# Kernel optimization log

Measured on AMD Instinct MI355X. Metric: run time of the kernel, lower is better.

The kernel has to match this reference:

```python
import jax, jax.numpy as jnp
import numpy as np
from jax import lax

DIM = 192
HEADS = 4
HEAD_DIM = DIM // HEADS
B, H, W = 4, 256, 256
EPS = 1e-12


def _conv(x, w, groups=1):
    # NCHW / OIHW, stride 1, SAME padding
    return lax.conv_general_dilated(
        x, w, window_strides=(1, 1), padding='SAME',
        feature_group_count=groups,
        dimension_numbers=('NCHW', 'OIHW', 'NCHW'))


def setup_inputs() -> dict:
    key = jax.random.key(0)
    k1, k2, k3, k4 = jax.random.split(key, 4)
    x = jax.random.normal(k1, (B, DIM, H, W), dtype=jnp.float32)
    qkv_w = jax.random.normal(k2, (3 * DIM, DIM, 1, 1), dtype=jnp.float32) * (1.0 / np.sqrt(DIM))
    dw_w = jax.random.normal(k3, (3 * DIM, 1, 3, 3), dtype=jnp.float32) * (1.0 / 3.0)
    proj_w = jax.random.normal(k4, (DIM, DIM, 1, 1), dtype=jnp.float32) * (1.0 / np.sqrt(DIM))
    temperature = jnp.ones((HEADS, 1, 1), dtype=jnp.float32)
    return {'x': x, 'qkv_w': qkv_w, 'dw_w': dw_w, 'proj_w': proj_w,
            'temperature': temperature}


def reference(x, qkv_w, dw_w, proj_w, temperature):
    b, c, h, w = x.shape
    qkv = _conv(x, qkv_w)                    # [b, 3c, h, w] 1x1 conv
    qkv = _conv(qkv, dw_w, groups=3 * c)     # depthwise 3x3
    q, k, v = jnp.split(qkv, 3, axis=1)      # each [b, c, h, w]
    hw = h * w
    q = q.reshape(b, HEADS, HEAD_DIM, hw)
    k = k.reshape(b, HEADS, HEAD_DIM, hw)
    v = v.reshape(b, HEADS, HEAD_DIM, hw)
    # L2-normalize over spatial dim (F.normalize, eps=1e-12 via clamp_min)
    q = q / jnp.maximum(jnp.linalg.norm(q, axis=3, keepdims=True), EPS)
    k = k / jnp.maximum(jnp.linalg.norm(k, axis=3, keepdims=True), EPS)
    # channel-wise attention: [b, heads, head_dim, head_dim]
    attn = jnp.einsum('bhdn,bhen->bhde', q, k) * temperature[None]
    attn = jax.nn.softmax(attn, axis=3)
    out = jnp.einsum('bhde,bhen->bhdn', attn, v)  # [b, heads, head_dim, hw]
    out = out.reshape(b, c, h, w)
    return _conv(out, proj_w)
```

## Files before the change

kernel.cpp:

```cpp
#include <hip/hip_runtime.h>
#include <hip/hip_bf16.h>

#define BATCH 4
#define CDIM 192
#define HWDIM 65536
#define IMGW 256
#define NHEADS 4
#define HDIM 48
#define KPAD 200

typedef __attribute__((ext_vector_type(8))) short short8;
typedef __attribute__((ext_vector_type(4))) float f32x4;

#define MFMA16(a, b, c) __builtin_amdgcn_mfma_f32_16x16x32_bf16(a, b, c, 0, 0, 0)

__device__ __forceinline__ ushort f2bf(float x) {
    unsigned u = __float_as_uint(x);
    unsigned r = u + 0x7FFFu + ((u >> 16) & 1u);
    return (ushort)(r >> 16);
}
__device__ __forceinline__ float bf2f(ushort h) {
    return __uint_as_float(((unsigned)h) << 16);
}

__global__ __launch_bounds__(256) void wsplit(
    const float* __restrict__ in, ushort* __restrict__ hi, ushort* __restrict__ lo, int n)
{
    int i = blockIdx.x * 256 + threadIdx.x;
    if (i < n) {
        float x = in[i];
        ushort h = f2bf(x);
        hi[i] = h;
        lo[i] = f2bf(x - bf2f(h));
    }
}

template<bool SPLITOUT>
__global__ __launch_bounds__(256) void gemm_staged(
    const ushort* __restrict__ Ahi, const ushort* __restrict__ Alo,
    const float*  __restrict__ X,
    ushort* __restrict__ qk_out,
    float*  __restrict__ v_out,
    float*  __restrict__ plain)
{
    __shared__ __align__(16) ushort Bh[64][KPAD];
    __shared__ __align__(16) ushort Bl[64][KPAD];

    const int t    = threadIdx.x;
    const int lane = t & 63;
    const int wave = t >> 6;
    const int n0   = blockIdx.x * 64;
    const int mw   = blockIdx.y * 192 + wave * 48;
    const int ar   = lane & 15;
    const int kg   = (lane >> 4) * 8;

    {
        const int n4 = (t & 15) * 4;
        const int kb = (t >> 4) * 2;
#pragma unroll
        for (int pass = 0; pass < 6; ++pass) {
            const int k2 = pass * 32 + kb;
            float4 f0 = *(const float4*)(X + (size_t)k2 * HWDIM + n0 + n4);
            float4 f1 = *(const float4*)(X + (size_t)(k2 + 1) * HWDIM + n0 + n4);
            const float* a0 = (const float*)&f0;
            const float* a1 = (const float*)&f1;
#pragma unroll
            for (int i = 0; i < 4; ++i) {
                ushort h0 = f2bf(a0[i]);
                ushort l0 = f2bf(a0[i] - bf2f(h0));
                ushort h1 = f2bf(a1[i]);
                ushort l1 = f2bf(a1[i] - bf2f(h1));
                *(unsigned*)&Bh[n4 + i][k2] = (unsigned)h0 | ((unsigned)h1 << 16);
                *(unsigned*)&Bl[n4 + i][k2] = (unsigned)l0 | ((unsigned)l1 << 16);
            }
        }
    }
    __syncthreads();

    f32x4 acc[3][4];
#pragma unroll
    for (int i = 0; i < 3; ++i)
#pragma unroll
        for (int j = 0; j < 4; ++j) { f32x4 z = {0.f, 0.f, 0.f, 0.f}; acc[i][j] = z; }

    const ushort* aph = Ahi + (size_t)(mw + ar) * 192 + kg;
    const ushort* apl = Alo + (size_t)(mw + ar) * 192 + kg;

#pragma unroll
    for (int k0 = 0; k0 < 192; k0 += 32) {
        short8 ah[3], al[3], bh[4], bl[4];
#pragma unroll
        for (int i = 0; i < 3; ++i) {
            ah[i] = *reinterpret_cast<const short8*>(aph + i * 16 * 192 + k0);
            al[i] = *reinterpret_cast<const short8*>(apl + i * 16 * 192 + k0);
        }
#pragma unroll
        for (int j = 0; j < 4; ++j) {
            bh[j] = *reinterpret_cast<const short8*>(&Bh[j * 16 + ar][k0 + kg]);
            bl[j] = *reinterpret_cast<const short8*>(&Bl[j * 16 + ar][k0 + kg]);
        }
#pragma unroll
        for (int i = 0; i < 3; ++i)
#pragma unroll
            for (int j = 0; j < 4; ++j) {
                acc[i][j] = MFMA16(ah[i], bh[j], acc[i][j]);
                acc[i][j] = MFMA16(ah[i], bl[j], acc[i][j]);
                acc[i][j] = MFMA16(al[i], bh[j], acc[i][j]);
            }
    }

    const int rr = (lane >> 4) * 4;
#pragma unroll
    for (int i = 0; i < 3; ++i)
#pragma unroll
        for (int j = 0; j < 4; ++j) {
            const int n = n0 + j * 16 + (lane & 15);
#pragma unroll
            for (int r = 0; r < 4; ++r) {
                const int mm = mw + i * 16 + rr + r;
                const float v = acc[i][j][r];
                if (SPLITOUT) {
                    if (mm < 384) qk_out[(size_t)mm * HWDIM + n] = f2bf(v);
                    else          v_out[(size_t)(mm - 384) * HWDIM + n] = v;
                } else {
                    plain[(size_t)mm * HWDIM + n] = v;
                }
            }
        }
}

__global__ __launch_bounds__(256) void dw3x3_bf(
    const ushort* __restrict__ in,
    const float* __restrict__ wdw,
    ushort* __restrict__ out)
{
    const int ch = blockIdx.x;
    const int y0 = blockIdx.y * 8;
    const int x  = threadIdx.x;
    __shared__ float rows[10][258];
    const ushort* inc = in + (size_t)ch * HWDIM;
#pragma unroll
    for (int r = 0; r < 10; ++r) {
        const int y = y0 - 1 + r;
        rows[r][x + 1] = (y >= 0 && y < IMGW) ? bf2f(inc[y * IMGW + x]) : 0.f;
    }
    if (x < 10) { rows[x][0] = 0.f; rows[x][257] = 0.f; }
    __syncthreads();
    float w[9];
#pragma unroll
    for (int i = 0; i < 9; ++i) w[i] = wdw[ch * 9 + i];
#pragma unroll
    for (int r = 0; r < 8; ++r) {
        float s = 0.f;
#pragma unroll
        for (int dy = 0; dy < 3; ++dy)
#pragma unroll
            for (int dx = 0; dx < 3; ++dx)
                s = fmaf(rows[r + dy][x + dx], w[dy * 3 + dx], s);
        out[(size_t)ch * HWDIM + (y0 + r) * IMGW + x] = f2bf(s);
    }
}

__global__ __launch_bounds__(256) void dw3x3_f32(
    const float* __restrict__ in,
    const float* __restrict__ wdw,
    float* __restrict__ out)
{
    const int ch = blockIdx.x;
    const int y0 = blockIdx.y * 8;
    const int x  = threadIdx.x;
    __shared__ float rows[10][258];
    const float* inc = in + (size_t)ch * HWDIM;
#pragma unroll
    for (int r = 0; r < 10; ++r) {
        const int y = y0 - 1 + r;
        rows[r][x + 1] = (y >= 0 && y < IMGW) ? inc[y * IMGW + x] : 0.f;
    }
    if (x < 10) { rows[x][0] = 0.f; rows[x][257] = 0.f; }
    __syncthreads();
    float w[9];
#pragma unroll
    for (int i = 0; i < 9; ++i) w[i] = wdw[ch * 9 + i];
#pragma unroll
    for (int r = 0; r < 8; ++r) {
        float s = 0.f;
#pragma unroll
        for (int dy = 0; dy < 3; ++dy)
#pragma unroll
            for (int dx = 0; dx < 3; ++dx)
                s = fmaf(rows[r + dy][x + dx], w[dy * 3 + dx], s);
        out[(size_t)ch * HWDIM + (y0 + r) * IMGW + x] = s;
    }
}

__global__ __launch_bounds__(256) void gram_mfma(
    const ushort* __restrict__ qk,
    float* __restrict__ Sb)
{
    const int h = blockIdx.y;
    const int lane = threadIdx.x & 63;
    const int wave = threadIdx.x >> 6;
    const int nbase = blockIdx.x * 2048 + wave * 512;
    const ushort* q0  = qk + (size_t)(h * HDIM) * HWDIM;
    const ushort* k0p = qk + (size_t)(192 + h * HDIM) * HWDIM;
    const int ar = lane & 15;
    const int kg = (lane >> 4) * 8;

    f32x4 acc[3][3];
#pragma unroll
    for (int i = 0; i < 3; ++i)
#pragma unroll
        for (int j = 0; j < 3; ++j) { f32x4 z = {0.f, 0.f, 0.f, 0.f}; acc[i][j] = z; }
    float sq[3] = {0.f, 0.f, 0.f}, sk[3] = {0.f, 0.f, 0.f};

    for (int ks = 0; ks < 512; ks += 32) {
        const int n = nbase + ks + kg;
        short8 qa[3], ka[3];
#pragma unroll
        for (int i = 0; i < 3; ++i) {
            qa[i] = *reinterpret_cast<const short8*>(q0  + (size_t)(i * 16 + ar) * HWDIM + n);
            ka[i] = *reinterpret_cast<const short8*>(k0p + (size_t)(i * 16 + ar) * HWDIM + n);
        }
#pragma unroll
        for (int i = 0; i < 3; ++i)
#pragma unroll
            for (int e = 0; e < 8; ++e) {
                float fq = bf2f((ushort)qa[i][e]);
                float fk = bf2f((ushort)ka[i][e]);
                sq[i] = fmaf(fq, fq, sq[i]);
                sk[i] = fmaf(fk, fk, sk[i]);
            }
#pragma unroll
        for (int i = 0; i < 3; ++i)
#pragma unroll
            for (int j = 0; j < 3; ++j)
                acc[i][j] = MFMA16(qa[i], ka[j], acc[i][j]);
    }

    __shared__ float S_l[2400];
    for (int t = threadIdx.x; t < 2400; t += 256) S_l[t] = 0.f;
    __syncthreads();
    const int rr = (lane >> 4) * 4;
#pragma unroll
    for (int i = 0; i < 3; ++i)
#pragma unroll
        for (int j = 0; j < 3; ++j)
#pragma unroll
            for (int r = 0; r < 4; ++r)
                atomicAdd(&S_l[(i * 16 + rr + r) * 48 + (j * 16 + ar)], acc[i][j][r]);
#pragma unroll
    for (int i = 0; i < 3; ++i) {
        sq[i] += __shfl_xor(sq[i], 16); sq[i] += __shfl_xor(sq[i], 32);
        sk[i] += __shfl_xor(sk[i], 16); sk[i] += __shfl_xor(sk[i], 32);
    }
    if ((lane >> 4) == 0) {
#pragma unroll
        for (int i = 0; i < 3; ++i) {
            atomicAdd(&S_l[2304 + i * 16 + ar], sq[i]);
            atomicAdd(&S_l[2352 + i * 16 + ar], sk[i]);
        }
    }
    __syncthreads();
    float* Sg = Sb + h * 2400;
    for (int t = threadIdx.x; t < 2400; t += 256) atomicAdd(&Sg[t], S_l[t]);
}

__global__ __launch_bounds__(256) void attn_w2(
    const float* __restrict__ S,
    const float* __restrict__ proj,
    const float* __restrict__ temp,
    ushort* __restrict__ W2hi,
    ushort* __restrict__ W2lo)
{
    __shared__ float attn[NHEADS][HDIM][HDIM];
    __shared__ float nqs[NHEADS][HDIM], nks[NHEADS][HDIM];
    const int t = threadIdx.x;
    const int co0 = blockIdx.x * 48;
    for (int idx = t; idx < NHEADS * 96; idx += 256) {
        const int h = idx / 96, r = idx % 96;
        float v = sqrtf(S[h * 2400 + 2304 + r]);
        v = fmaxf(v, 1e-12f);
        if (r < 48) nqs[h][r] = v; else nks[h][r - 48] = v;
    }
    __syncthreads();
    if (t < NHEADS * HDIM) {
        const int h = t / HDIM, d = t % HDIM;
        const float tp  = temp[h];
        const float inq = 1.0f / nqs[h][d];
        float row[48];
        float mx = -1e30f;
#pragma unroll
        for (int e = 0; e < 48; ++e) {
            row[e] = S[h * 2400 + d * 48 + e] * inq / nks[h][e] * tp;
            mx = fmaxf(mx, row[e]);
        }
        float sum = 0.f;
#pragma unroll
        for (int e = 0; e < 48; ++e) { row[e] = expf(row[e] - mx); sum += row[e]; }
        const float isum = 1.0f / sum;
#pragma unroll
        for (int e = 0; e < 48; ++e) attn[h][d][e] = row[e] * isum;
    }
    __syncthreads();
    for (int idx = t; idx < 48 * 192; idx += 256) {
        const int co = co0 + idx / 192, he = idx % 192;
        const int h = he / 48, e = he % 48;
        const float* pr = proj + co * 192 + h * 48;
        float s = 0.f;
#pragma unroll
        for (int d = 0; d < 48; ++d) s = fmaf(pr[d], attn[h][d][e], s);
        ushort hh = f2bf(s);
        W2hi[co * 192 + he] = hh;
        W2lo[co * 192 + he] = f2bf(s - bf2f(hh));
    }
}

__global__ void zerof(float* __restrict__ p, int n)
{
    const int i = blockIdx.x * 256 + threadIdx.x;
    if (i < n) p[i] = 0.f;
}

extern "C" void kernel_launch(void* const* d_in, const int* in_sizes, int n_in,
                              void* d_out, int out_size, void* d_ws, size_t ws_size,
                              hipStream_t stream)
{
    const float* x      = (const float*)d_in[0];
    const float* qkv_w  = (const float*)d_in[1];
    const float* dw_w   = (const float*)d_in[2];
    const float* proj_w = (const float*)d_in[3];
    const float* temp   = (const float*)d_in[4];
    float* out = (float*)d_out;

    char* w = (char*)d_ws;
    ushort* qk_pre = (ushort*)w;                 w += (size_t)384 * HWDIM * 2;
    float*  v_pre  = (float*)w;                  w += (size_t)192 * HWDIM * 4;
    ushort* qk_dw  = (ushort*)w;                 w += (size_t)384 * HWDIM * 2;
    float*  v_dw   = (float*)w;                  w += (size_t)192 * HWDIM * 4;
    ushort* A1hi   = (ushort*)w;                 w += (size_t)576 * 192 * 2;
    ushort* A1lo   = (ushort*)w;                 w += (size_t)576 * 192 * 2;
    ushort* W2hi   = (ushort*)w;                 w += (size_t)192 * 192 * 2;
    ushort* W2lo   = (ushort*)w;                 w += (size_t)192 * 192 * 2;
    float*  S_all  = (float*)w;                  w += (size_t)BATCH * 4 * 2400 * 4;

    zerof<<<150, 256, 0, stream>>>(S_all, BATCH * 4 * 2400);
    wsplit<<<(576 * 192 + 255) / 256, 256, 0, stream>>>(qkv_w, A1hi, A1lo, 576 * 192);

    for (int b = 0; b < BATCH; ++b) {
        const float* xb = x   + (size_t)b * CDIM * HWDIM;
        float*       ob = out + (size_t)b * CDIM * HWDIM;
        float*       Sb = S_all + (size_t)b * 4 * 2400;

        gemm_staged<true><<<dim3(1024, 3), 256, 0, stream>>>(
            A1hi, A1lo, xb, qk_pre, v_pre, nullptr);
        dw3x3_bf <<<dim3(384, 32), 256, 0, stream>>>(qk_pre, dw_w, qk_dw);
        dw3x3_f32<<<dim3(192, 32), 256, 0, stream>>>(v_pre, dw_w + 384 * 9, v_dw);
        gram_mfma<<<dim3(32, 4), 256, 0, stream>>>(qk_dw, Sb);
        attn_w2<<<4, 256, 0, stream>>>(Sb, proj_w, temp, W2hi, W2lo);
        gemm_staged<false><<<dim3(1024, 1), 256, 0, stream>>>(
            W2hi, W2lo, v_dw, nullptr, nullptr, ob);
    }
}
```

Before: 1.256 ms.

## Batch two images per launch, swizzle GEMM LDS, vectorize depthwise conv

The pipeline now runs two batch images per launch through a z grid dimension, which halves the launch count and gives the small kernels (gram, attn_w2, proj GEMM) twice as many blocks. The GEMM's shared-memory B tile is stored with an XOR swizzle on 8-element chunks to reduce bank conflicts on the short8 reads. The two depthwise conv kernels become one template that loads with float4/ushort4 and computes a 4x4 output patch per thread over 16-row tiles. The cost is doubled workspace for intermediates.

New measurement: 1.078 ms. 14.2% less time.

```diff
diff --git a/kernel.cpp b/kernel.cpp
--- a/kernel.cpp
+++ b/kernel.cpp
@@ -2,6 +2,7 @@
 #include <hip/hip_bf16.h>
 
 #define BATCH 4
+#define ZPAIR 2
 #define CDIM 192
 #define HWDIM 65536
 #define IMGW 256
@@ -41,12 +42,14 @@
     const float*  __restrict__ X,
     ushort* __restrict__ qk_out,
     float*  __restrict__ v_out,
-    float*  __restrict__ plain)
-{
-    __shared__ __align__(16) ushort Bh[64][KPAD];
-    __shared__ __align__(16) ushort Bl[64][KPAD];
+    float*  __restrict__ plain,
+    int zAStride)
+{
+    __shared__ __align__(16) ushort Bh[64 * KPAD];
+    __shared__ __align__(16) ushort Bl[64 * KPAD];
 
     const int t    = threadIdx.x;
+    const int z    = blockIdx.z;
     const int lane = t & 63;
     const int wave = t >> 6;
     const int n0   = blockIdx.x * 64;
@@ -54,24 +57,30 @@
     const int ar   = lane & 15;
     const int kg   = (lane >> 4) * 8;
 
+    const float* Xz = X + (size_t)z * CDIM * HWDIM;
+
     {
         const int n4 = (t & 15) * 4;
         const int kb = (t >> 4) * 2;
 #pragma unroll
         for (int pass = 0; pass < 6; ++pass) {
             const int k2 = pass * 32 + kb;
-            float4 f0 = *(const float4*)(X + (size_t)k2 * HWDIM + n0 + n4);
-            float4 f1 = *(const float4*)(X + (size_t)(k2 + 1) * HWDIM + n0 + n4);
+            float4 f0 = *(const float4*)(Xz + (size_t)k2 * HWDIM + n0 + n4);
+            float4 f1 = *(const float4*)(Xz + (size_t)(k2 + 1) * HWDIM + n0 + n4);
             const float* a0 = (const float*)&f0;
             const float* a1 = (const float*)&f1;
+            const int cb = k2 >> 3;
+            const int ki = k2 & 7;
 #pragma unroll
             for (int i = 0; i < 4; ++i) {
+                const int row = n4 + i;
+                const int off = row * KPAD + ((cb ^ ((row >> 2) & 7)) << 3) + ki;
                 ushort h0 = f2bf(a0[i]);
                 ushort l0 = f2bf(a0[i] - bf2f(h0));
                 ushort h1 = f2bf(a1[i]);
                 ushort l1 = f2bf(a1[i] - bf2f(h1));
-                *(unsigned*)&Bh[n4 + i][k2] = (unsigned)h0 | ((unsigned)h1 << 16);
-                *(unsigned*)&Bl[n4 + i][k2] = (unsigned)l0 | ((unsigned)l1 << 16);
+                *(unsigned*)&Bh[off] = (unsigned)h0 | ((unsigned)h1 << 16);
+                *(unsigned*)&Bl[off] = (unsigned)l0 | ((unsigned)l1 << 16);
             }
         }
     }
@@ -81,10 +90,10 @@
 #pragma unroll
     for (int i = 0; i < 3; ++i)
 #pragma unroll
-        for (int j = 0; j < 4; ++j) { f32x4 z = {0.f, 0.f, 0.f, 0.f}; acc[i][j] = z; }
-
-    const ushort* aph = Ahi + (size_t)(mw + ar) * 192 + kg;
-    const ushort* apl = Alo + (size_t)(mw + ar) * 192 + kg;
+        for (int j = 0; j < 4; ++j) { f32x4 zz = {0.f, 0.f, 0.f, 0.f}; acc[i][j] = zz; }
+
+    const ushort* aph = Ahi + (size_t)z * zAStride + (size_t)(mw + ar) * 192 + kg;
+    const ushort* apl = Alo + (size_t)z * zAStride + (size_t)(mw + ar) * 192 + kg;
 
 #pragma unroll
     for (int k0 = 0; k0 < 192; k0 += 32) {
@@ -94,10 +103,13 @@
             ah[i] = *reinterpret_cast<const short8*>(aph + i * 16 * 192 + k0);
             al[i] = *reinterpret_cast<const short8*>(apl + i * 16 * 192 + k0);
         }
+        const int cb = (k0 + kg) >> 3;
 #pragma unroll
         for (int j = 0; j < 4; ++j) {
-            bh[j] = *reinterpret_cast<const short8*>(&Bh[j * 16 + ar][k0 + kg]);
-            bl[j] = *reinterpret_cast<const short8*>(&Bl[j * 16 + ar][k0 + kg]);
+            const int row = j * 16 + ar;
+            const int off = row * KPAD + ((cb ^ ((row >> 2) & 7)) << 3);
+            bh[j] = *reinterpret_cast<const short8*>(&Bh[off]);
+            bl[j] = *reinterpret_cast<const short8*>(&Bl[off]);
         }
 #pragma unroll
         for (int i = 0; i < 3; ++i)
@@ -120,76 +132,85 @@
                 const int mm = mw + i * 16 + rr + r;
                 const float v = acc[i][j][r];
                 if (SPLITOUT) {
-                    if (mm < 384) qk_out[(size_t)mm * HWDIM + n] = f2bf(v);
-                    else          v_out[(size_t)(mm - 384) * HWDIM + n] = v;
+                    if (mm < 384)
+                        qk_out[(size_t)z * 384 * HWDIM + (size_t)mm * HWDIM + n] = f2bf(v);
+                    else
+                        v_out[(size_t)z * CDIM * HWDIM + (size_t)(mm - 384) * HWDIM + n] = v;
                 } else {
-                    plain[(size_t)mm * HWDIM + n] = v;
+                    plain[(size_t)z * CDIM * HWDIM + (size_t)mm * HWDIM + n] = v;
                 }
             }
         }
 }
 
-__global__ __launch_bounds__(256) void dw3x3_bf(
-    const ushort* __restrict__ in,
+template<bool BF>
+__global__ __launch_bounds__(256) void dw3x3(
+    const void* __restrict__ in_,
     const float* __restrict__ wdw,
-    ushort* __restrict__ out)
-{
+    void* __restrict__ out_, int nch)
+{
+    __shared__ float rows[18][264];
+    const int t  = threadIdx.x;
     const int ch = blockIdx.x;
-    const int y0 = blockIdx.y * 8;
-    const int x  = threadIdx.x;
-    __shared__ float rows[10][258];
-    const ushort* inc = in + (size_t)ch * HWDIM;
-#pragma unroll
-    for (int r = 0; r < 10; ++r) {
-        const int y = y0 - 1 + r;
-        rows[r][x + 1] = (y >= 0 && y < IMGW) ? bf2f(inc[y * IMGW + x]) : 0.f;
-    }
-    if (x < 10) { rows[x][0] = 0.f; rows[x][257] = 0.f; }
-    __syncthreads();
+    const int y0 = blockIdx.y * 16;
+    const int z  = blockIdx.z;
+    const size_t base = ((size_t)z * nch + ch) * HWDIM;
+
+    for (int idx = t; idx < 18 * 64; idx += 256) {
+        const int row = idx >> 6;
+        const int c4  = (idx & 63) << 2;
+        const int y   = y0 - 1 + row;
+        float4 v = {0.f, 0.f, 0.f, 0.f};
+        if (y >= 0 && y < IMGW) {
+            if (BF) {
+                const ushort* p = (const ushort*)in_ + base + (size_t)y * IMGW + c4;
+                ushort4 u = *(const ushort4*)p;
+                v.x = bf2f(u.x); v.y = bf2f(u.y); v.z = bf2f(u.z); v.w = bf2f(u.w);
+            } else {
+                v = *(const float4*)((const float*)in_ + base + (size_t)y * IMGW + c4);
+            }
+        }
+        *(float4*)&rows[row][4 + c4] = v;
+    }
+    if (t < 18) { rows[t][3] = 0.f; rows[t][260] = 0.f; }
+    __syncthreads();
+
     float w[9];
 #pragma unroll
     for (int i = 0; i < 9; ++i) w[i] = wdw[ch * 9 + i];
-#pragma unroll
-    for (int r = 0; r < 8; ++r) {
-        float s = 0.f;
-#pragma unroll
-        for (int dy = 0; dy < 3; ++dy)
-#pragma unroll
-            for (int dx = 0; dx < 3; ++dx)
-                s = fmaf(rows[r + dy][x + dx], w[dy * 3 + dx], s);
-        out[(size_t)ch * HWDIM + (y0 + r) * IMGW + x] = f2bf(s);
-    }
-}
-
-__global__ __launch_bounds__(256) void dw3x3_f32(
-    const float* __restrict__ in,
-    const float* __restrict__ wdw,
-    float* __restrict__ out)
-{
-    const int ch = blockIdx.x;
-    const int y0 = blockIdx.y * 8;
-    const int x  = threadIdx.x;
-    __shared__ float rows[10][258];
-    const float* inc = in + (size_t)ch * HWDIM;
-#pragma unroll
-    for (int r = 0; r < 10; ++r) {
-        const int y = y0 - 1 + r;
-        rows[r][x + 1] = (y >= 0 && y < IMGW) ? inc[y * IMGW + x] : 0.f;
-    }
-    if (x < 10) { rows[x][0] = 0.f; rows[x][257] = 0.f; }
-    __syncthreads();
-    float w[9];
-#pragma unroll
-    for (int i = 0; i < 9; ++i) w[i] = wdw[ch * 9 + i];
-#pragma unroll
-    for (int r = 0; r < 8; ++r) {
-        float s = 0.f;
-#pragma unroll
-        for (int dy = 0; dy < 3; ++dy)
-#pragma unroll
-            for (int dx = 0; dx < 3; ++dx)
-                s = fmaf(rows[r + dy][x + dx], w[dy * 3 + dx], s);
-        out[(size_t)ch * HWDIM + (y0 + r) * IMGW + x] = s;
+
+    const int rg = t >> 6;
+    const int cg = t & 63;
+    float win[6][6];
+#pragma unroll
+    for (int r6 = 0; r6 < 6; ++r6) {
+        const int row = rg * 4 + r6;
+        float4 mid = *(const float4*)&rows[row][4 + cg * 4];
+        win[r6][0] = rows[row][3 + cg * 4];
+        win[r6][1] = mid.x; win[r6][2] = mid.y; win[r6][3] = mid.z; win[r6][4] = mid.w;
+        win[r6][5] = rows[row][8 + cg * 4];
+    }
+#pragma unroll
+    for (int rr = 0; rr < 4; ++rr) {
+        float o[4];
+#pragma unroll
+        for (int cc = 0; cc < 4; ++cc) {
+            float s = 0.f;
+#pragma unroll
+            for (int dy = 0; dy < 3; ++dy)
+#pragma unroll
+                for (int dx = 0; dx < 3; ++dx)
+                    s = fmaf(win[rr + dy][cc + dx], w[dy * 3 + dx], s);
+            o[cc] = s;
+        }
+        const size_t oo = base + (size_t)(y0 + rg * 4 + rr) * IMGW + cg * 4;
+        if (BF) {
+            ushort4 u;
+            u.x = f2bf(o[0]); u.y = f2bf(o[1]); u.z = f2bf(o[2]); u.w = f2bf(o[3]);
+            *(ushort4*)((ushort*)out_ + oo) = u;
+        } else {
+            *(float4*)((float*)out_ + oo) = make_float4(o[0], o[1], o[2], o[3]);
+        }
     }
 }
 
@@ -198,11 +219,12 @@
     float* __restrict__ Sb)
 {
     const int h = blockIdx.y;
+    const int z = blockIdx.z;
     const int lane = threadIdx.x & 63;
     const int wave = threadIdx.x >> 6;
     const int nbase = blockIdx.x * 2048 + wave * 512;
-    const ushort* q0  = qk + (size_t)(h * HDIM) * HWDIM;
-    const ushort* k0p = qk + (size_t)(192 + h * HDIM) * HWDIM;
+    const ushort* q0  = qk + (size_t)z * 384 * HWDIM + (size_t)(h * HDIM) * HWDIM;
+    const ushort* k0p = q0 + (size_t)CDIM * HWDIM;
     const int ar = lane & 15;
     const int kg = (lane >> 4) * 8;
 
@@ -210,7 +232,7 @@
 #pragma unroll
     for (int i = 0; i < 3; ++i)
 #pragma unroll
-        for (int j = 0; j < 3; ++j) { f32x4 z = {0.f, 0.f, 0.f, 0.f}; acc[i][j] = z; }
+        for (int j = 0; j < 3; ++j) { f32x4 zz = {0.f, 0.f, 0.f, 0.f}; acc[i][j] = zz; }
     float sq[3] = {0.f, 0.f, 0.f}, sk[3] = {0.f, 0.f, 0.f};
 
     for (int ks = 0; ks < 512; ks += 32) {
@@ -261,12 +283,12 @@
         }
     }
     __syncthreads();
-    float* Sg = Sb + h * 2400;
+    float* Sg = Sb + (size_t)z * 4 * 2400 + h * 2400;
     for (int t = threadIdx.x; t < 2400; t += 256) atomicAdd(&Sg[t], S_l[t]);
 }
 
 __global__ __launch_bounds__(256) void attn_w2(
-    const float* __restrict__ S,
+    const float* __restrict__ S_all,
     const float* __restrict__ proj,
     const float* __restrict__ temp,
     ushort* __restrict__ W2hi,
@@ -276,6 +298,11 @@
     __shared__ float nqs[NHEADS][HDIM], nks[NHEADS][HDIM];
     const int t = threadIdx.x;
     const int co0 = blockIdx.x * 48;
+    const int z = blockIdx.y;
+    const float* S = S_all + (size_t)z * 4 * 2400;
+    ushort* w2h = W2hi + (size_t)z * CDIM * CDIM;
+    ushort* w2l = W2lo + (size_t)z * CDIM * CDIM;
+
     for (int idx = t; idx < NHEADS * 96; idx += 256) {
         const int h = idx / 96, r = idx % 96;
         float v = sqrtf(S[h * 2400 + 2304 + r]);
@@ -310,8 +337,8 @@
 #pragma unroll
         for (int d = 0; d < 48; ++d) s = fmaf(pr[d], attn[h][d][e], s);
         ushort hh = f2bf(s);
-        W2hi[co * 192 + he] = hh;
-        W2lo[co * 192 + he] = f2bf(s - bf2f(hh));
+        w2h[co * 192 + he] = hh;
+        w2l[co * 192 + he] = f2bf(s - bf2f(hh));
     }
 }
 
@@ -333,31 +360,31 @@
     float* out = (float*)d_out;
 
     char* w = (char*)d_ws;
-    ushort* qk_pre = (ushort*)w;                 w += (size_t)384 * HWDIM * 2;
-    float*  v_pre  = (float*)w;                  w += (size_t)192 * HWDIM * 4;
-    ushort* qk_dw  = (ushort*)w;                 w += (size_t)384 * HWDIM * 2;
-    float*  v_dw   = (float*)w;                  w += (size_t)192 * HWDIM * 4;
-    ushort* A1hi   = (ushort*)w;                 w += (size_t)576 * 192 * 2;
-    ushort* A1lo   = (ushort*)w;                 w += (size_t)576 * 192 * 2;
-    ushort* W2hi   = (ushort*)w;                 w += (size_t)192 * 192 * 2;
-    ushort* W2lo   = (ushort*)w;                 w += (size_t)192 * 192 * 2;
-    float*  S_all  = (float*)w;                  w += (size_t)BATCH * 4 * 2400 * 4;
+    ushort* qk_pre = (ushort*)w;  w += (size_t)ZPAIR * 384 * HWDIM * 2;
+    float*  v_pre  = (float*)w;   w += (size_t)ZPAIR * CDIM * HWDIM * 4;
+    ushort* qk_dw  = (ushort*)w;  w += (size_t)ZPAIR * 384 * HWDIM * 2;
+    float*  v_dw   = (float*)w;   w += (size_t)ZPAIR * CDIM * HWDIM * 4;
+    ushort* A1hi   = (ushort*)w;  w += (size_t)576 * 192 * 2;
+    ushort* A1lo   = (ushort*)w;  w += (size_t)576 * 192 * 2;
+    ushort* W2hi   = (ushort*)w;  w += (size_t)ZPAIR * CDIM * CDIM * 2;
+    ushort* W2lo   = (ushort*)w;  w += (size_t)ZPAIR * CDIM * CDIM * 2;
+    float*  S_all  = (float*)w;   w += (size_t)BATCH * 4 * 2400 * 4;
 
     zerof<<<150, 256, 0, stream>>>(S_all, BATCH * 4 * 2400);
     wsplit<<<(576 * 192 + 255) / 256, 256, 0, stream>>>(qkv_w, A1hi, A1lo, 576 * 192);
 
-    for (int b = 0; b < BATCH; ++b) {
-        const float* xb = x   + (size_t)b * CDIM * HWDIM;
-        float*       ob = out + (size_t)b * CDIM * HWDIM;
-        float*       Sb = S_all + (size_t)b * 4 * 2400;
-
-        gemm_staged<true><<<dim3(1024, 3), 256, 0, stream>>>(
-            A1hi, A1lo, xb, qk_pre, v_pre, nullptr);
-        dw3x3_bf <<<dim3(384, 32), 256, 0, stream>>>(qk_pre, dw_w, qk_dw);
-        dw3x3_f32<<<dim3(192, 32), 256, 0, stream>>>(v_pre, dw_w + 384 * 9, v_dw);
-        gram_mfma<<<dim3(32, 4), 256, 0, stream>>>(qk_dw, Sb);
-        attn_w2<<<4, 256, 0, stream>>>(Sb, proj_w, temp, W2hi, W2lo);
-        gemm_staged<false><<<dim3(1024, 1), 256, 0, stream>>>(
-            W2hi, W2lo, v_dw, nullptr, nullptr, ob);
-    }
-}
+    for (int p = 0; p < BATCH / ZPAIR; ++p) {
+        const float* xp = x   + (size_t)p * ZPAIR * CDIM * HWDIM;
+        float*       op = out + (size_t)p * ZPAIR * CDIM * HWDIM;
+        float*       Sp = S_all + (size_t)p * ZPAIR * 4 * 2400;
+
+        gemm_staged<true><<<dim3(1024, 3, ZPAIR), 256, 0, stream>>>(
+            A1hi, A1lo, xp, qk_pre, v_pre, nullptr, 0);
+        dw3x3<true> <<<dim3(384, 16, ZPAIR), 256, 0, stream>>>(qk_pre, dw_w, qk_dw, 384);
+        dw3x3<false><<<dim3(192, 16, ZPAIR), 256, 0, stream>>>(v_pre, dw_w + 384 * 9, v_dw, 192);
+        gram_mfma<<<dim3(32, 4, ZPAIR), 256, 0, stream>>>(qk_dw, Sp);
+        attn_w2<<<dim3(4, ZPAIR), 256, 0, stream>>>(Sp, proj_w, temp, W2hi, W2lo);
+        gemm_staged<false><<<dim3(1024, 1, ZPAIR), 256, 0, stream>>>(
+            W2hi, W2lo, v_dw, nullptr, nullptr, op, CDIM * CDIM);
+    }
+}
```
